# Optimization experiments

Measured on AMD Instinct MI355X. Metric: run time of the kernel, lower is better.

The kernel has to match this reference:

```python
import jax, jax.numpy as jnp
import numpy as np

NUM_USERS = 100000
NUM_ITEMS = 50000
NUM_HIDDEN = 64
NUM_BINS = 10
BATCH = 131072
N_QUAD = 64  # quadrature nodes in incomplete/complete beta
EPS = 1e-6


def _trapz0(y, dt):
    # trapezoidal rule along axis 0 with uniform spacing dt
    return (jnp.sum(y, axis=0) - 0.5 * (y[0] + y[-1])) * dt


def setup_inputs() -> dict:
    key = jax.random.key(0)
    ks = jax.random.split(key, 12)
    return {
        "uid_input": jax.random.randint(ks[0], (BATCH,), 0, NUM_USERS),
        "iid_input": jax.random.randint(ks[1], (BATCH,), 0, NUM_ITEMS),
        "uid_features": 0.1 * jax.random.normal(ks[2], (NUM_USERS, NUM_HIDDEN + 1), jnp.float32),
        "iid_features": 0.1 * jax.random.normal(ks[3], (NUM_ITEMS, NUM_HIDDEN + 1), jnp.float32),
        "uid_bin_terms": 0.1 * jax.random.normal(ks[4], (NUM_USERS, NUM_BINS), jnp.float32),
        "iid_bin_terms": 0.1 * jax.random.normal(ks[5], (NUM_ITEMS, NUM_BINS), jnp.float32),
        "uid_alpha_emb": 0.01 * jax.random.normal(ks[6], (NUM_USERS, 1), jnp.float32),
        "uid_beta_emb": 0.01 * jax.random.normal(ks[7], (NUM_USERS, 1), jnp.float32),
        "iid_alpha_emb": 0.01 * jax.random.normal(ks[8], (NUM_ITEMS, 1), jnp.float32),
        "iid_beta_emb": 0.01 * jax.random.normal(ks[9], (NUM_ITEMS, 1), jnp.float32),
        "global_bias": jnp.asarray(2.0, jnp.float32),
    }


def reference(uid_input, iid_input, uid_features, iid_features,
              uid_bin_terms, iid_bin_terms, uid_alpha_emb, uid_beta_emb,
              iid_alpha_emb, iid_beta_emb, global_bias):
    # embedding lookups (confidence features alias the regular features)
    uf = uid_features[uid_input]          # (B, H+1)
    vf = iid_features[iid_input]          # (B, H+1)
    u = uf[:, :-1]                        # (B, H)
    v = vf[:, :-1]

    # mu / upsilon (upsilon_layer_id == 2: |dot|)
    dot = jnp.sum(u * v, axis=-1, keepdims=True)                    # (B, 1)
    len_prod = (jnp.linalg.norm(u, axis=1, keepdims=True)
                * jnp.linalg.norm(v, axis=1, keepdims=True))
    mu = jnp.clip(0.5 + 0.5 * dot / jnp.maximum(len_prod, EPS), EPS, 1.0 - EPS)
    upsilon = jnp.maximum(jnp.abs(dot), EPS)

    # alpha / beta
    alpha = jnp.maximum(0.01, mu * upsilon)
    beta = jnp.maximum(0.01, upsilon - alpha)
    alpha = global_bias + alpha
    beta = global_bias + beta
    alpha = jnp.maximum(0.01, alpha + uid_alpha_emb[uid_input] + iid_alpha_emb[iid_input])  # (B,1)
    beta = jnp.maximum(0.01, beta + uid_beta_emb[uid_input] + iid_beta_emb[iid_input])      # (B,1)

    # per-pair bin edges via normalized exp + cumsum
    terms = jnp.exp(uid_bin_terms[uid_input] + iid_bin_terms[iid_input])  # (B, NUM_BINS)
    terms = terms / jnp.sum(terms, axis=-1, keepdims=True)
    edges = jnp.cumsum(terms, axis=-1)                                    # (B, NUM_BINS)

    # regularized incomplete beta at interior edges via trapezoidal quadrature
    x = edges[:, :-1]                                  # (B, NB-1)
    t = jnp.linspace(0.0, 1.0, N_QUAD, dtype=alpha.dtype)
    dt = t[1] - t[0]
    t3 = t[:, None, None]                              # (n, 1, 1)
    a3 = alpha[None, :, :]                             # (1, B, 1)
    b3 = beta[None, :, :]
    tx = t3 * x[None]                                  # (n, B, NB-1)
    integrand = (tx ** (a3 - 1.0)) * ((1.0 - tx) ** (b3 - 1.0))
    integrand = integrand * (t3 <= x[None]).astype(integrand.dtype)
    Bx_ab = _trapz0(integrand, dt)                     # (B, NB-1)

    # complete beta B(a, b)
    c_int = (t[None, :] ** (alpha - 1.0)) * ((1.0 - t[None, :]) ** (beta - 1.0))  # (B, n)
    B_ab = (jnp.sum(c_int, axis=-1) - 0.5 * (c_int[:, 0] + c_int[:, -1])) * dt    # (B,)

    cdf = Bx_ab / B_ab[:, None]                        # (B, NB-1)
    cdf = jnp.concatenate([cdf, jnp.ones_like(alpha)], axis=-1)  # (B, NB)
    mass = jnp.concatenate([cdf[:, :1], cdf[:, 1:] - cdf[:, :-1]], axis=-1)
    return mass
```

## Files before the change

kernel.cpp:

```cpp
#include <hip/hip_runtime.h>
#include <math.h>

#define BLOCK 256
#define SPB (BLOCK / 4)

struct F4a4 { float a, b, c, d; };

__device__ __forceinline__ float exp2_fast(float x) {
#if __has_builtin(__builtin_amdgcn_exp2f)
    return __builtin_amdgcn_exp2f(x);
#else
    return __expf(x * 0.69314718055994531f);
#endif
}

__device__ __forceinline__ double exp_f64_fast(double x) {
    const double L2E = 1.4426950408889634074;
    const double LN2 = 0.69314718055994530942;
    double n = rint(x * L2E);
    double r = fma(x, L2E, -n);
    double w = r * LN2;
    double p = 2.08767569878680989792e-9;
    p = fma(p, w, 2.50521083854417187751e-8);
    p = fma(p, w, 2.75573192239858906526e-7);
    p = fma(p, w, 2.75573192239858925110e-6);
    p = fma(p, w, 2.48015873015873015873e-5);
    p = fma(p, w, 1.98412698412698412698e-4);
    p = fma(p, w, 1.38888888888888888889e-3);
    p = fma(p, w, 8.33333333333333333333e-3);
    p = fma(p, w, 4.16666666666666666667e-2);
    p = fma(p, w, 1.66666666666666666667e-1);
    p = fma(p, w, 0.5);
    p = fma(p, w, 1.0);
    p = fma(p, w, 1.0);
    const double sc = __longlong_as_double((long long)(1023 + (int)n) << 52);
    return p * sc;
}

__global__ __launch_bounds__(BLOCK) void lbd_kernel(
    const int* __restrict__ uid_in, const int* __restrict__ iid_in,
    const float* __restrict__ uf,  const float* __restrict__ vf,
    const float* __restrict__ ubt, const float* __restrict__ ibt,
    const float* __restrict__ uae, const float* __restrict__ ube,
    const float* __restrict__ iae, const float* __restrict__ ibe,
    const float* __restrict__ gbp, float* __restrict__ out, int B)
{
    __shared__ float2 s_num[64];
    __shared__ float2 s_den[64];
    const int tid = threadIdx.x;
    if (tid < 64) {
        const double STEP0 = 1.0 / 63.0;
        float tf = (float)((double)tid * STEP0);
        if (tid == 63) tf = 1.0f;
        const float lt = __log2f(tf);
        const float l1 = __log2f(1.0f - tf);
        s_num[tid] = make_float2(tf, lt);
        s_den[tid] = make_float2(lt, l1);
    }
    __syncthreads();

    const int sub = tid & 3;
    const int s0  = blockIdx.x * SPB + (tid >> 2);
    const bool valid = (s0 < B);
    const int s = valid ? s0 : (B - 1);

    const int u = uid_in[s];
    const int v = iid_in[s];

    const float* pu = uf + (long long)u * 65;
    const float* pv = vf + (long long)v * 65;
    float dotp = 0.f, sup = 0.f, svp = 0.f;
#pragma unroll
    for (int c = 0; c < 4; ++c) {
        const F4a4 a = *(const F4a4*)(pu + c * 16 + sub * 4);
        const F4a4 b = *(const F4a4*)(pv + c * 16 + sub * 4);
        dotp += a.a * b.a + a.b * b.b + a.c * b.c + a.d * b.d;
        sup  += a.a * a.a + a.b * a.b + a.c * a.c + a.d * a.d;
        svp  += b.a * b.a + b.b * b.b + b.c * b.c + b.d * b.d;
    }
#pragma unroll
    for (int d = 1; d < 4; d <<= 1) {
        dotp += __shfl_xor(dotp, d, 64);
        sup  += __shfl_xor(sup,  d, 64);
        svp  += __shfl_xor(svp,  d, 64);
    }

    float emb;
    {
        const float* ep = (sub == 0) ? (uae + u)
                        : (sub == 1) ? (iae + v)
                        : (sub == 2) ? (ube + u)
                        :              (ibe + v);
        emb = *ep;
    }
    const float ua_ = __shfl(emb, 0, 4);
    const float ia_ = __shfl(emb, 1, 4);
    const float ub_ = __shfl(emb, 2, 4);
    const float ib_ = __shfl(emb, 3, 4);

    const float gb = gbp[0];
    const float len_prod = sqrtf(sup) * sqrtf(svp);
    const float EPS = 1e-6f;
    const float HI  = (float)(1.0 - 1e-6);
    float mu = 0.5f + (0.5f * dotp) / fmaxf(len_prod, EPS);
    mu = fminf(fmaxf(mu, EPS), HI);
    const float ups = fmaxf(fabsf(dotp), EPS);
    const float al0 = fmaxf(0.01f, mu * ups);
    const float be0 = fmaxf(0.01f, ups - al0);
    const float alpha = fmaxf(0.01f, ((gb + al0) + ua_) + ia_);
    const float beta  = fmaxf(0.01f, ((gb + be0) + ub_) + ib_);
    const float am1 = alpha - 1.0f;
    const float bm1 = beta  - 1.0f;

    const double STEP = 1.0 / 63.0;
    const int lb = 3 * sub;
    double e0, e1 = 0.0, e2 = 0.0;
    {
        const long long ur = (long long)u * 10, vr = (long long)v * 10;
        const int i1 = (lb + 1 <= 9) ? lb + 1 : 9;
        const int i2 = (lb + 2 <= 9) ? lb + 2 : 9;
        e0 = exp_f64_fast((double)ubt[ur + lb] + (double)ibt[vr + lb]);
        const double t1 = exp_f64_fast((double)ubt[ur + i1] + (double)ibt[vr + i1]);
        const double t2 = exp_f64_fast((double)ubt[ur + i2] + (double)ibt[vr + i2]);
        if (lb + 1 <= 9) e1 = t1;
        if (lb + 2 <= 9) e2 = t2;
    }
    const double c0 = e0, c1 = c0 + e1, c2 = c1 + e2;
    double p = c2;
#pragma unroll
    for (int d = 1; d < 4; d <<= 1) {
        const double t = __shfl_up(p, d, 4);
        if (sub >= d) p += t;
    }
    const double ssum = __shfl(p, 3, 4);
    const double rsum = 1.0 / ssum;
    const double ex   = p - c2;
    float xf_own[3] = {0.f, 0.f, 0.f}, lx_own[3] = {0.f, 0.f, 0.f};
    int   im_own[3] = {0, 0, 0};
    const double cg0 = ex + c0, cg1 = ex + c1, cg2 = ex + c2;
#pragma unroll
    for (int r = 0; r < 3; ++r) {
        const double cgr = (r == 0) ? cg0 : (r == 1) ? cg1 : cg2;
        if (lb + r <= 8) {
            const double x = cgr * rsum;
            int k = (int)(x * 63.0);
            k = (k > 62) ? 62 : k;
            const int dec = ((double)k * STEP > x) ? 1 : 0;
            const int inc = ((k < 62) && ((double)(k + 1) * STEP <= x)) ? 1 : 0;
            im_own[r] = k + inc - dec;
            xf_own[r] = (float)x;
            lx_own[r] = __log2f(xf_own[r]);
        }
    }

    float xfj[9], alxj[9];
    int   imj[9], Mw[9];
#pragma unroll
    for (int j = 0; j < 9; ++j) {
        const int src  = j / 3;
        const int slot = j % 3;
        const float xo = (slot == 0) ? xf_own[0] : (slot == 1) ? xf_own[1] : xf_own[2];
        const float lo = (slot == 0) ? lx_own[0] : (slot == 1) ? lx_own[1] : lx_own[2];
        const int   io = (slot == 0) ? im_own[0] : (slot == 1) ? im_own[1] : im_own[2];
        xfj[j]  = __shfl(xo, src, 4);
        alxj[j] = am1 * __shfl(lo, src, 4);
        imj[j]  = __shfl(io, src, 4);
        int mm = imj[j];
        mm = max(mm, __shfl_xor(mm, 4, 64));
        mm = max(mm, __shfl_xor(mm, 8, 64));
        mm = max(mm, __shfl_xor(mm, 16, 64));
        mm = max(mm, __shfl_xor(mm, 32, 64));
        Mw[j] = __builtin_amdgcn_readfirstlane((mm >> 2) + 1);
    }

    float accD = 0.f;
#pragma unroll
    for (int m = 0; m < 16; ++m) {
        const float2 dd = s_den[m * 4 + sub];
        accD += exp2_fast(fmaf(bm1, dd.y, am1 * dd.x));
    }

    float acc[9];
#pragma unroll
    for (int j = 0; j < 9; ++j) {
        const float xj  = xfj[j];
        const float axj = alxj[j];
        const int   imv = imj[j];
        const int   M2  = (Mw[j] + 1) & ~1;
        float a0 = 0.f, a1 = 0.f;
        for (int m = 0; m < M2; m += 2) {
            const int i0 = m * 4 + sub;
            const int i1 = i0 + 4;
            const float2 t0 = s_num[i0];
            const float2 t1 = s_num[i1];
            const float w0 = fmaf(-t0.x, xj, 1.0f);
            const float w1 = fmaf(-t1.x, xj, 1.0f);
            const float e0v = fmaf(bm1, __log2f(w0), fmaf(am1, t0.y, axj));
            const float e1v = fmaf(bm1, __log2f(w1), fmaf(am1, t1.y, axj));
            const float y0 = exp2_fast(e0v);
            const float y1 = exp2_fast(e1v);
            a0 += ((unsigned)(i0 - 1) < (unsigned)imv) ? y0 : 0.f;
            a1 += ((unsigned)(i1 - 1) < (unsigned)imv) ? y1 : 0.f;
        }
        acc[j] = a0 + a1;
    }

#pragma unroll
    for (int d = 1; d < 4; d <<= 1) {
        accD += __shfl_xor(accD, d, 64);
#pragma unroll
        for (int j = 0; j < 9; ++j) acc[j] += __shfl_xor(acc[j], d, 64);
    }

    const float dtf = (float)(1.0 / 63.0);
    const float rB  = 1.0f / (accD * dtf);
    float cdfv[9];
#pragma unroll
    for (int j = 0; j < 9; ++j) cdfv[j] = (acc[j] * dtf) * rB;

    const float o0 = (sub == 0) ? cdfv[0]
                   : (sub == 1) ? (cdfv[1] - cdfv[0])
                   : (sub == 2) ? (cdfv[2] - cdfv[1])
                   :              (cdfv[3] - cdfv[2]);
    const float o1 = (sub == 0) ? (cdfv[4] - cdfv[3])
                   : (sub == 1) ? (cdfv[5] - cdfv[4])
                   : (sub == 2) ? (cdfv[6] - cdfv[5])
                   :              (cdfv[7] - cdfv[6]);
    const float o2 = (sub == 0) ? (cdfv[8] - cdfv[7])
                   :              (1.0f - cdfv[8]);
    if (valid) {
        const long long ob = (long long)s * 10;
        out[ob + sub]     = o0;
        out[ob + 4 + sub] = o1;
        if (sub < 2) out[ob + 8 + sub] = o2;
    }
}

extern "C" void kernel_launch(void* const* d_in, const int* in_sizes, int n_in,
                              void* d_out, int out_size, void* d_ws, size_t ws_size,
                              hipStream_t stream) {
    (void)n_in; (void)out_size; (void)d_ws; (void)ws_size;
    const int*   uid = (const int*)d_in[0];
    const int*   iid = (const int*)d_in[1];
    const float* uf  = (const float*)d_in[2];
    const float* vf  = (const float*)d_in[3];
    const float* ubt = (const float*)d_in[4];
    const float* ibt = (const float*)d_in[5];
    const float* uae = (const float*)d_in[6];
    const float* ube = (const float*)d_in[7];
    const float* iae = (const float*)d_in[8];
    const float* ibe = (const float*)d_in[9];
    const float* gb  = (const float*)d_in[10];
    float* out = (float*)d_out;
    const int B = in_sizes[0];
    const int grid = (B + SPB - 1) / SPB;
    hipLaunchKernelGGL(lbd_kernel, dim3(grid), dim3(BLOCK), 0, stream,
                       uid, iid, uf, vf, ubt, ibt, uae, ube, iae, ibe, gb, out, B);
}
```

Before: 125.8 us.

## Batch quadrature over four bin edges per loop and shift node indices

Restructures the incomplete-beta quadrature so that each loop iteration evaluates four bin edges at once. Each node's shared-memory value and its am1*log(t) term are loaded or computed once and reused across those four edges, and the next node pair is prefetched. Node indexing is shifted by one so the t=0 node is skipped, and the shared tables are padded so reads past the last node stay in bounds. The ninth edge is handled in a fully unrolled 16-step loop together with the complete-beta denominator. The price is higher register pressure, and grouped edges now share one trip count, taken from the largest edge in each group.

Measured after the change: 122.7 us. -2.5%, faster.

```diff
diff --git a/kernel.cpp b/kernel.cpp
--- a/kernel.cpp
+++ b/kernel.cpp
@@ -45,17 +45,15 @@
     const float* __restrict__ iae, const float* __restrict__ ibe,
     const float* __restrict__ gbp, float* __restrict__ out, int B)
 {
-    __shared__ float2 s_num[64];
-    __shared__ float2 s_den[64];
+    __shared__ float2 s_num[76];
+    __shared__ float2 s_den[68];
     const int tid = threadIdx.x;
-    if (tid < 64) {
+    if (tid < 76) {
         const double STEP0 = 1.0 / 63.0;
-        float tf = (float)((double)tid * STEP0);
-        if (tid == 63) tf = 1.0f;
+        float tf = (tid >= 63) ? 1.0f : (float)((double)tid * STEP0);
         const float lt = __log2f(tf);
-        const float l1 = __log2f(1.0f - tf);
         s_num[tid] = make_float2(tf, lt);
-        s_den[tid] = make_float2(lt, l1);
+        if (tid < 68) s_den[tid] = make_float2(lt, __log2f(1.0f - tf));
     }
     __syncthreads();
 
@@ -170,40 +168,96 @@
         mm = max(mm, __shfl_xor(mm, 8, 64));
         mm = max(mm, __shfl_xor(mm, 16, 64));
         mm = max(mm, __shfl_xor(mm, 32, 64));
-        Mw[j] = __builtin_amdgcn_readfirstlane((mm >> 2) + 1);
-    }
-
-    float accD = 0.f;
-#pragma unroll
-    for (int m = 0; m < 16; ++m) {
-        const float2 dd = s_den[m * 4 + sub];
-        accD += exp2_fast(fmaf(bm1, dd.y, am1 * dd.x));
-    }
+        Mw[j] = __builtin_amdgcn_readfirstlane((mm + 3) >> 2);
+    }
+
+    const float2 P0 = s_num[sub + 1];
+    const float2 P1 = s_num[sub + 5];
 
     float acc[9];
-#pragma unroll
-    for (int j = 0; j < 9; ++j) {
-        const float xj  = xfj[j];
-        const float axj = alxj[j];
-        const int   imv = imj[j];
-        const int   M2  = (Mw[j] + 1) & ~1;
-        float a0 = 0.f, a1 = 0.f;
-        for (int m = 0; m < M2; m += 2) {
-            const int i0 = m * 4 + sub;
-            const int i1 = i0 + 4;
-            const float2 t0 = s_num[i0];
-            const float2 t1 = s_num[i1];
-            const float w0 = fmaf(-t0.x, xj, 1.0f);
-            const float w1 = fmaf(-t1.x, xj, 1.0f);
-            const float e0v = fmaf(bm1, __log2f(w0), fmaf(am1, t0.y, axj));
-            const float e1v = fmaf(bm1, __log2f(w1), fmaf(am1, t1.y, axj));
-            const float y0 = exp2_fast(e0v);
-            const float y1 = exp2_fast(e1v);
-            a0 += ((unsigned)(i0 - 1) < (unsigned)imv) ? y0 : 0.f;
-            a1 += ((unsigned)(i1 - 1) < (unsigned)imv) ? y1 : 0.f;
+
+#define QUAD_LOOP(j0)                                                              \
+    {                                                                              \
+        const float x0 = xfj[j0],     x1 = xfj[j0 + 1];                            \
+        const float x2 = xfj[j0 + 2], x3 = xfj[j0 + 3];                            \
+        const float g0 = alxj[j0],     g1 = alxj[j0 + 1];                          \
+        const float g2 = alxj[j0 + 2], g3 = alxj[j0 + 3];                          \
+        const int   k0 = imj[j0],     k1 = imj[j0 + 1];                            \
+        const int   k2 = imj[j0 + 2], k3 = imj[j0 + 3];                            \
+        const int   M  = Mw[j0 + 3];                      \
+        float A00 = 0.f, A01 = 0.f, A10 = 0.f, A11 = 0.f;                          \
+        float A20 = 0.f, A21 = 0.f, A30 = 0.f, A31 = 0.f;                          \
+        float2 t0 = P0, t1 = P1;                                                   \
+        int m = 0;                                                                 \
+        for (; m + 2 <= M; m += 2) {                                               \
+            const float2 n0 = s_num[(m + 2) * 4 + sub + 1];                        \
+            const float2 n1 = s_num[(m + 3) * 4 + sub + 1];                        \
+            const int i0 = m * 4 + sub + 1;                                        \
+            const int i1 = i0 + 4;                                                 \
+            const float h0 = fmaf(am1, t0.y, 0.f);              \
+            const float h1 = fmaf(am1, t1.y, 0.f);                                 \
+            const float lw0 = __log2f(fmaf(-t0.x, x0, 1.0f));                      \
+            const float lw1 = __log2f(fmaf(-t0.x, x1, 1.0f));                      \
+            const float lw2 = __log2f(fmaf(-t0.x, x2, 1.0f));                      \
+            const float lw3 = __log2f(fmaf(-t0.x, x3, 1.0f));                      \
+            const float mw0 = __log2f(fmaf(-t1.x, x0, 1.0f));                      \
+            const float mw1 = __log2f(fmaf(-t1.x, x1, 1.0f));                      \
+            const float mw2 = __log2f(fmaf(-t1.x, x2, 1.0f));                      \
+            const float mw3 = __log2f(fmaf(-t1.x, x3, 1.0f));                      \
+            const float y00 = exp2_fast(fmaf(bm1, lw0, h0 + g0));                  \
+            const float y10 = exp2_fast(fmaf(bm1, lw1, h0 + g1));                  \
+            const float y20 = exp2_fast(fmaf(bm1, lw2, h0 + g2));                  \
+            const float y30 = exp2_fast(fmaf(bm1, lw3, h0 + g3));                  \
+            const float y01 = exp2_fast(fmaf(bm1, mw0, h1 + g0));                  \
+            const float y11 = exp2_fast(fmaf(bm1, mw1, h1 + g1));                  \
+            const float y21 = exp2_fast(fmaf(bm1, mw2, h1 + g2));                  \
+            const float y31 = exp2_fast(fmaf(bm1, mw3, h1 + g3));                  \
+            A00 += (i0 <= k0) ? y00 : 0.f;  A01 += (i1 <= k0) ? y01 : 0.f;         \
+            A10 += (i0 <= k1) ? y10 : 0.f;  A11 += (i1 <= k1) ? y11 : 0.f;         \
+            A20 += (i0 <= k2) ? y20 : 0.f;  A21 += (i1 <= k2) ? y21 : 0.f;         \
+            A30 += (i0 <= k3) ? y30 : 0.f;  A31 += (i1 <= k3) ? y31 : 0.f;         \
+            t0 = n0; t1 = n1;                                                      \
+        }                                                                          \
+        if (m < M) {                                                               \
+            const int i0 = m * 4 + sub + 1;                                        \
+            const float h0 = fmaf(am1, t0.y, 0.f);                                 \
+            const float lw0 = __log2f(fmaf(-t0.x, x0, 1.0f));                      \
+            const float lw1 = __log2f(fmaf(-t0.x, x1, 1.0f));                      \
+            const float lw2 = __log2f(fmaf(-t0.x, x2, 1.0f));                      \
+            const float lw3 = __log2f(fmaf(-t0.x, x3, 1.0f));                      \
+            A00 += (i0 <= k0) ? exp2_fast(fmaf(bm1, lw0, h0 + g0)) : 0.f;          \
+            A10 += (i0 <= k1) ? exp2_fast(fmaf(bm1, lw1, h0 + g1)) : 0.f;          \
+            A20 += (i0 <= k2) ? exp2_fast(fmaf(bm1, lw2, h0 + g2)) : 0.f;          \
+            A30 += (i0 <= k3) ? exp2_fast(fmaf(bm1, lw3, h0 + g3)) : 0.f;          \
+        }                                                                          \
+        acc[j0]     = A00 + A01;  acc[j0 + 1] = A10 + A11;                         \
+        acc[j0 + 2] = A20 + A21;  acc[j0 + 3] = A30 + A31;                         \
+    }
+
+    QUAD_LOOP(0)
+    QUAD_LOOP(4)
+#undef QUAD_LOOP
+
+
+    float accD = 0.f, a80 = 0.f, a81 = 0.f;
+    {
+        const float xj  = xfj[8];
+        const float axj = alxj[8];
+        const int   imv = imj[8];
+#pragma unroll
+        for (int m = 0; m < 16; ++m) {
+            const int i = m * 4 + sub + 1;
+            const float2 tn = s_num[i];
+            const float2 dn = s_den[i];
+            accD += exp2_fast(fmaf(bm1, dn.y, am1 * dn.x));
+            const float w = fmaf(-tn.x, xj, 1.0f);
+            const float e = fmaf(bm1, __log2f(w), fmaf(am1, tn.y, axj));
+            const float y = exp2_fast(e);
+            if ((m & 1) == 0) a80 += (i <= imv) ? y : 0.f;
+            else              a81 += (i <= imv) ? y : 0.f;
         }
-        acc[j] = a0 + a1;
-    }
+    }
+    acc[8] = a80 + a81;
 
 #pragma unroll
     for (int d = 1; d < 4; d <<= 1) {
```
